# Kernel tuning notes

Hardware: AMD Instinct MI355X
Metric: run time of the kernel (lower is better)

Reference implementation:

```python
import jax, jax.numpy as jnp
import numpy as np
from jax import lax

WIN = 9
LOSS_WEIGHT = 1.0

def _box_sum(x, win):
    return lax.reduce_window(x, 0.0, lax.add,
                             window_dimensions=(1, 1, win, win, win),
                             window_strides=(1, 1, 1, 1, 1),
                             padding='SAME')

def setup_inputs() -> dict:
    key = jax.random.key(0)
    k1, k2 = jax.random.split(key)
    shape = (2, 1, 160, 192, 160)
    predict = jax.random.uniform(k1, shape, dtype=jnp.float32)
    target = jax.random.uniform(k2, shape, dtype=jnp.float32)
    return {"predict": predict, "target": target}

def reference(predict, target):
    Ii, Ji = target, predict
    win = WIN
    win_size = float(win ** 3)

    I_sum = _box_sum(Ii, win)
    J_sum = _box_sum(Ji, win)
    I2_sum = _box_sum(Ii * Ii, win)
    J2_sum = _box_sum(Ji * Ji, win)
    IJ_sum = _box_sum(Ii * Ji, win)

    u_I = I_sum / win_size
    u_J = J_sum / win_size
    cross = IJ_sum - u_J * I_sum - u_I * J_sum + u_I * u_J * win_size
    I_var = I2_sum - 2.0 * u_I * I_sum + u_I * u_I * win_size
    J_var = J2_sum - 2.0 * u_J * J_sum + u_J * u_J * win_size
    cc = cross * cross / (I_var * J_var + 1e-05)
    loss = 1.0 - jnp.mean(cc)
    return loss * LOSS_WEIGHT
```

## Files before the change

kernel.cpp:

```cpp
#include <hip/hip_runtime.h>
#include <hip/hip_fp16.h>


#define NX 160
#define NY 192
#define NZ 160
#define NB 2
#define SLICE (NX * NY)
#define VOL   (SLICE * NZ)
#define TOTAL (VOL * NB)

#define TX 32
#define TY 16
#define ZC 5
#define GXT (NX / TX)
#define GYT (NY / TY)
#define GZT (NZ / ZC)
#define NBLK (GXT * GYT * GZT * NB)

#define HY 24
#define ZRS 40
#define ZQQ (HY * ZRS + 8)
#define RRS 40
#define RQQ (HY * RRS + 8)
#define SRS 40
#define SQQ (TY * SRS + 8)
#define INV729 (1.0f / 729.0f)

__device__ __forceinline__ void lds_barrier() {
    asm volatile("s_waitcnt lgkmcnt(0)" ::: "memory");
    __builtin_amdgcn_s_barrier();
}

__device__ __forceinline__ float4 f4add(float4 a, float4 b) {
    return make_float4(a.x + b.x, a.y + b.y, a.z + b.z, a.w + b.w);
}
__device__ __forceinline__ float4 f4sub(float4 a, float4 b) {
    return make_float4(a.x - b.x, a.y - b.y, a.z - b.z, a.w - b.w);
}
__device__ __forceinline__ float4 f4mul(float4 a, float4 b) {
    return make_float4(a.x * b.x, a.y * b.y, a.z * b.z, a.w * b.w);
}

union U8 { uint4 u; __half2 h[4]; };

__device__ __forceinline__ U8 ld8(const __half* p) {
    U8 r; r.u = *(const uint4*)p; return r;
}
__device__ __forceinline__ void st8(__half* p, const U8& v) {
    *(uint4*)p = v.u;
}

__global__ __launch_bounds__(256) void ncc_main(
    const float* __restrict__ J_pred,
    const float* __restrict__ I_targ,
    float* __restrict__ partial)
{
    const int tid = threadIdx.x;

    const int lin = blockIdx.x;
    const int s   = (lin & 7) * (NBLK / 8) + (lin >> 3);
    const int bx  = s % GXT;
    const int r1  = s / GXT;
    const int by  = r1 % GYT;
    const int r2  = r1 / GYT;
    const int zc  = r2 % GZT;
    const int b   = r2 / GZT;

    const int x0 = bx * TX;
    const int y0 = by * TY;
    const int z0 = zc * ZC;

    __shared__ __align__(16) __half Zq[5 * ZQQ];
    __shared__ __align__(16) __half Rq[5 * RQQ];
    __shared__ float redbuf[4];
    __half* const Sq = Zq;

    const bool is_col = (tid < 240);
    const int  crow = tid / 10;
    const int  cxg  = tid - crow * 10;
    const int  gy = y0 - 4 + crow;
    const int  gx = x0 - 4 + cxg * 4;
    const bool vxy = is_col && ((unsigned)gy < (unsigned)NY) && (gx >= 0) && (gx <= NX - 4);
    const size_t cbase = (size_t)b * VOL + (vxy ? (size_t)(gy * NX + gx) : 0);
    const float* const baseI = I_targ + cbase;
    const float* const baseJ = J_pred + cbase;

    const float4 f40 = make_float4(0.f, 0.f, 0.f, 0.f);
    float4 rS0 = f40, rS1 = f40, rS2 = f40, rS3 = f40, rS4 = f40;

#pragma unroll 3
    for (int ss = 0; ss < 9; ++ss) {
        const int z = z0 - 5 + ss;
        float4 aI = f40, aJ = f40;
        if (vxy && (unsigned)z < (unsigned)NZ) {
            aI = *(const float4*)(baseI + (size_t)z * SLICE);
            aJ = *(const float4*)(baseJ + (size_t)z * SLICE);
        }
        rS0 = f4add(rS0, aI);
        rS1 = f4add(rS1, aJ);
        rS2 = f4add(rS2, f4mul(aI, aI));
        rS3 = f4add(rS3, f4mul(aJ, aJ));
        rS4 = f4add(rS4, f4mul(aI, aJ));
    }

    float4 nIa = f40, nJa = f40, nIs = f40, nJs = f40;
    if (vxy) {
        const int za = z0 + 4;
        nIa = *(const float4*)(baseI + (size_t)za * SLICE);
        nJa = *(const float4*)(baseJ + (size_t)za * SLICE);
        const int zs = z0 - 5;
        if (zs >= 0) {
            nIs = *(const float4*)(baseI + (size_t)zs * SLICE);
            nJs = *(const float4*)(baseJ + (size_t)zs * SLICE);
        }
    }

    const int ty  = tid >> 4;
    const int tx2 = tid & 15;
    float acc = 0.f;

#pragma unroll 1
    for (int so = 0; so < ZC; ++so) {
        rS0 = f4add(rS0, f4sub(nIa, nIs));
        rS1 = f4add(rS1, f4sub(nJa, nJs));
        rS2 = f4add(rS2, f4sub(f4mul(nIa, nIa), f4mul(nIs, nIs)));
        rS3 = f4add(rS3, f4sub(f4mul(nJa, nJa), f4mul(nJs, nJs)));
        rS4 = f4add(rS4, f4sub(f4mul(nIa, nJa), f4mul(nIs, nJs)));

        nIa = f40; nJa = f40; nIs = f40; nJs = f40;
        if (so < ZC - 1 && vxy) {
            const int za = z0 + 5 + so;
            if (za < NZ) {
                nIa = *(const float4*)(baseI + (size_t)za * SLICE);
                nJa = *(const float4*)(baseJ + (size_t)za * SLICE);
            }
            const int zs = z0 + so - 4;
            if (zs >= 0) {
                nIs = *(const float4*)(baseI + (size_t)zs * SLICE);
                nJs = *(const float4*)(baseJ + (size_t)zs * SLICE);
            }
        }

        if (is_col) {
            const int o = crow * ZRS + cxg * 4;
            union { uint2 u; __half2 h[2]; } pk;
            pk.h[0] = __float22half2_rn(make_float2(rS0.x, rS0.y));
            pk.h[1] = __float22half2_rn(make_float2(rS0.z, rS0.w));
            *(uint2*)&Zq[0 * ZQQ + o] = pk.u;
            pk.h[0] = __float22half2_rn(make_float2(rS1.x, rS1.y));
            pk.h[1] = __float22half2_rn(make_float2(rS1.z, rS1.w));
            *(uint2*)&Zq[1 * ZQQ + o] = pk.u;
            pk.h[0] = __float22half2_rn(make_float2(rS2.x, rS2.y));
            pk.h[1] = __float22half2_rn(make_float2(rS2.z, rS2.w));
            *(uint2*)&Zq[2 * ZQQ + o] = pk.u;
            pk.h[0] = __float22half2_rn(make_float2(rS3.x, rS3.y));
            pk.h[1] = __float22half2_rn(make_float2(rS3.z, rS3.w));
            *(uint2*)&Zq[3 * ZQQ + o] = pk.u;
            pk.h[0] = __float22half2_rn(make_float2(rS4.x, rS4.y));
            pk.h[1] = __float22half2_rn(make_float2(rS4.z, rS4.w));
            *(uint2*)&Zq[4 * ZQQ + o] = pk.u;
        }
        lds_barrier();

        if (tid < 240) {
            const int q   = tid / 48;
            const int rem = tid - q * 48;
            const int row = rem >> 1;
            const int h   = rem & 1;
            const __half* src = &Zq[q * ZQQ + row * ZRS + h * 16];
            float c[24];
#pragma unroll
            for (int g = 0; g < 3; ++g) {
                U8 v = ld8(src + g * 8);
#pragma unroll
                for (int j = 0; j < 4; ++j) {
                    const float2 f = __half22float2(v.h[j]);
                    c[g * 8 + j * 2 + 0] = f.x;
                    c[g * 8 + j * 2 + 1] = f.y;
                }
            }
            float sx = c[0] + c[1] + c[2] + c[3] + c[4]
                     + c[5] + c[6] + c[7] + c[8];
            float o[16];
            o[0] = sx;
#pragma unroll
            for (int i = 1; i < 16; ++i) { sx += c[i + 8] - c[i - 1]; o[i] = sx; }
            __half* dst = &Rq[q * RQQ + row * RRS + h * 16];
#pragma unroll
            for (int g = 0; g < 2; ++g) {
                U8 w;
#pragma unroll
                for (int j = 0; j < 4; ++j)
                    w.h[j] = __float22half2_rn(make_float2(o[g * 8 + j * 2],
                                                           o[g * 8 + j * 2 + 1]));
                st8(dst + g * 8, w);
            }
        }
        lds_barrier();

        if (tid < 80) {
            const int q  = tid / 16;
            const int rm = tid & 15;
            const int xg = rm >> 2;
            const int q4 = rm & 3;
            const __half* rb = &Rq[q * RQQ + (q4 * 4) * RRS + xg * 8];
            __half* sb = &Sq[q * SQQ + (q4 * 4) * SRS + xg * 8];
            U8 sum = ld8(rb);
#pragma unroll
            for (int k = 1; k < 9; ++k) {
                const U8 t = ld8(rb + k * RRS);
#pragma unroll
                for (int j = 0; j < 4; ++j) sum.h[j] = __hadd2(sum.h[j], t.h[j]);
            }
            st8(sb, sum);
#pragma unroll
            for (int i = 1; i < 4; ++i) {
                const U8 nw = ld8(rb + (i + 8) * RRS);
                const U8 od = ld8(rb + (i - 1) * RRS);
#pragma unroll
                for (int j = 0; j < 4; ++j)
                    sum.h[j] = __hadd2(sum.h[j], __hsub2(nw.h[j], od.h[j]));
                st8(sb + i * SRS, sum);
            }
        }
        lds_barrier();

        {
            const int o = ty * SRS + tx2 * 2;
            const float2 S0 = __half22float2(*(const __half2*)&Sq[0 * SQQ + o]);
            const float2 S1 = __half22float2(*(const __half2*)&Sq[1 * SQQ + o]);
            const float2 S2 = __half22float2(*(const __half2*)&Sq[2 * SQQ + o]);
            const float2 S3 = __half22float2(*(const __half2*)&Sq[3 * SQQ + o]);
            const float2 S4 = __half22float2(*(const __half2*)&Sq[4 * SQQ + o]);
            {
                const float cross = S4.x - S0.x * S1.x * INV729;
                const float Iv    = S2.x - S0.x * S0.x * INV729;
                const float Jv    = S3.x - S1.x * S1.x * INV729;
                acc += (cross * cross) / (Iv * Jv + 1e-5f);
            }
            {
                const float cross = S4.y - S0.y * S1.y * INV729;
                const float Iv    = S2.y - S0.y * S0.y * INV729;
                const float Jv    = S3.y - S1.y * S1.y * INV729;
                acc += (cross * cross) / (Iv * Jv + 1e-5f);
            }
        }
        lds_barrier();
    }

#pragma unroll
    for (int off = 32; off > 0; off >>= 1) acc += __shfl_down(acc, off);
    __syncthreads();
    if ((tid & 63) == 0) redbuf[tid >> 6] = acc;
    __syncthreads();
    if (tid == 0) partial[s] = redbuf[0] + redbuf[1] + redbuf[2] + redbuf[3];
}

__global__ __launch_bounds__(256) void ncc_final(
    const float* __restrict__ partial, float* __restrict__ out)
{
    __shared__ float sm[256];
    const int tid = threadIdx.x;
    float v = 0.f;
    for (int i = tid; i < NBLK; i += 256) v += partial[i];
    sm[tid] = v;
    __syncthreads();
#pragma unroll
    for (int w = 128; w > 0; w >>= 1) {
        if (tid < w) sm[tid] += sm[tid + w];
        __syncthreads();
    }
    if (tid == 0) out[0] = 1.0f - sm[0] * (1.0f / (float)TOTAL);
}

extern "C" void kernel_launch(void* const* d_in, const int* in_sizes, int n_in,
                              void* d_out, int out_size, void* d_ws, size_t ws_size,
                              hipStream_t stream)
{
    const float* predict = (const float*)d_in[0];
    const float* target  = (const float*)d_in[1];
    float* partial = (float*)d_ws;

    ncc_main<<<dim3(NBLK), 256, 0, stream>>>(predict, target, partial);
    ncc_final<<<1, 256, 0, stream>>>(partial, (float*)d_out);
}
```

Before: 59.99 us.

## Make z-sum and y-pass LDS staging wave-private to drop two block barriers

Each wave now owns six halo rows for the z-sum staging and four output rows for the y-pass, in a wave-private LDS region. This turns two of the four per-slice block barriers into wave-local lgkmcnt waits, keeping only the barrier around the shared x-pass buffer. The running z-sums of squares also switch to FMA and a difference-times-sum form to trim VALU work. The cost is more LDS footprint, and the result depends on lockstep execution within a wave for the private buffers to stay correct.

```diff
diff --git a/kernel.cpp b/kernel.cpp
--- a/kernel.cpp
+++ b/kernel.cpp
@@ -18,19 +18,24 @@
 #define GZT (NZ / ZC)
 #define NBLK (GXT * GYT * GZT * NB)
 
-#define HY 24
-#define ZRS 40
-#define ZQQ (HY * ZRS + 8)
+#define WROWS 6
+#define ZQS 48
+#define ZQP (WROWS * ZQS + 8)
+#define ZPRIV (5 * ZQP)
+#define ZPRIVP 1504
+#define SQS 40
+#define SQP (4 * SQS + 8)
 #define RRS 40
-#define RQQ (HY * RRS + 8)
-#define SRS 40
-#define SQQ (TY * SRS + 8)
+#define RQQ (24 * RRS + 8)
 #define INV729 (1.0f / 729.0f)
 
 __device__ __forceinline__ void lds_barrier() {
     asm volatile("s_waitcnt lgkmcnt(0)" ::: "memory");
     __builtin_amdgcn_s_barrier();
 }
+__device__ __forceinline__ void lds_fence() {
+    asm volatile("s_waitcnt lgkmcnt(0)" ::: "memory");
+}
 
 __device__ __forceinline__ float4 f4add(float4 a, float4 b) {
     return make_float4(a.x + b.x, a.y + b.y, a.z + b.z, a.w + b.w);
@@ -41,9 +46,12 @@
 __device__ __forceinline__ float4 f4mul(float4 a, float4 b) {
     return make_float4(a.x * b.x, a.y * b.y, a.z * b.z, a.w * b.w);
 }
+__device__ __forceinline__ float4 f4fma(float4 a, float4 b, float4 c) {
+    return make_float4(fmaf(a.x, b.x, c.x), fmaf(a.y, b.y, c.y),
+                       fmaf(a.z, b.z, c.z), fmaf(a.w, b.w, c.w));
+}
 
 union U8 { uint4 u; __half2 h[4]; };
-
 __device__ __forceinline__ U8 ld8(const __half* p) {
     U8 r; r.u = *(const uint4*)p; return r;
 }
@@ -56,7 +64,9 @@
     const float* __restrict__ I_targ,
     float* __restrict__ partial)
 {
-    const int tid = threadIdx.x;
+    const int tid  = threadIdx.x;
+    const int wave = tid >> 6;
+    const int lane = tid & 63;
 
     const int lin = blockIdx.x;
     const int s   = (lin & 7) * (NBLK / 8) + (lin >> 3);
@@ -71,16 +81,17 @@
     const int y0 = by * TY;
     const int z0 = zc * ZC;
 
-    __shared__ __align__(16) __half Zq[5 * ZQQ];
+    __shared__ __align__(16) __half ZS[4 * ZPRIVP];
     __shared__ __align__(16) __half Rq[5 * RQQ];
     __shared__ float redbuf[4];
-    __half* const Sq = Zq;
-
-    const bool is_col = (tid < 240);
-    const int  crow = tid / 10;
-    const int  cxg  = tid - crow * 10;
-    const int  gy = y0 - 4 + crow;
-    const int  gx = x0 - 4 + cxg * 4;
+    __half* const ZW = &ZS[wave * ZPRIVP];
+
+    const bool is_col = (lane < 60);
+    const int  rl  = lane / 10;
+    const int  xg  = lane - rl * 10;
+    const int  row = wave * WROWS + rl;
+    const int  gy  = y0 - 4 + row;
+    const int  gx  = x0 - 4 + xg * 4;
     const bool vxy = is_col && ((unsigned)gy < (unsigned)NY) && (gx >= 0) && (gx <= NX - 4);
     const size_t cbase = (size_t)b * VOL + (vxy ? (size_t)(gy * NX + gx) : 0);
     const float* const baseI = I_targ + cbase;
@@ -99,9 +110,9 @@
         }
         rS0 = f4add(rS0, aI);
         rS1 = f4add(rS1, aJ);
-        rS2 = f4add(rS2, f4mul(aI, aI));
-        rS3 = f4add(rS3, f4mul(aJ, aJ));
-        rS4 = f4add(rS4, f4mul(aI, aJ));
+        rS2 = f4fma(aI, aI, rS2);
+        rS3 = f4fma(aJ, aJ, rS3);
+        rS4 = f4fma(aI, aJ, rS4);
     }
 
     float4 nIa = f40, nJa = f40, nIs = f40, nJs = f40;
@@ -122,11 +133,15 @@
 
 #pragma unroll 1
     for (int so = 0; so < ZC; ++so) {
-        rS0 = f4add(rS0, f4sub(nIa, nIs));
-        rS1 = f4add(rS1, f4sub(nJa, nJs));
-        rS2 = f4add(rS2, f4sub(f4mul(nIa, nIa), f4mul(nIs, nIs)));
-        rS3 = f4add(rS3, f4sub(f4mul(nJa, nJa), f4mul(nJs, nJs)));
-        rS4 = f4add(rS4, f4sub(f4mul(nIa, nJa), f4mul(nIs, nJs)));
+        {
+            const float4 dI = f4sub(nIa, nIs), pI = f4add(nIa, nIs);
+            const float4 dJ = f4sub(nJa, nJs), pJ = f4add(nJa, nJs);
+            rS0 = f4add(rS0, dI);
+            rS1 = f4add(rS1, dJ);
+            rS2 = f4fma(dI, pI, rS2);
+            rS3 = f4fma(dJ, pJ, rS3);
+            rS4 = f4add(rS4, f4sub(f4mul(nIa, nJa), f4mul(nIs, nJs)));
+        }
 
         nIa = f40; nJa = f40; nIs = f40; nJs = f40;
         if (so < ZC - 1 && vxy) {
@@ -143,32 +158,31 @@
         }
 
         if (is_col) {
-            const int o = crow * ZRS + cxg * 4;
+            const int o = rl * ZQS + xg * 4;
             union { uint2 u; __half2 h[2]; } pk;
             pk.h[0] = __float22half2_rn(make_float2(rS0.x, rS0.y));
             pk.h[1] = __float22half2_rn(make_float2(rS0.z, rS0.w));
-            *(uint2*)&Zq[0 * ZQQ + o] = pk.u;
+            *(uint2*)&ZW[0 * ZQP + o] = pk.u;
             pk.h[0] = __float22half2_rn(make_float2(rS1.x, rS1.y));
             pk.h[1] = __float22half2_rn(make_float2(rS1.z, rS1.w));
-            *(uint2*)&Zq[1 * ZQQ + o] = pk.u;
+            *(uint2*)&ZW[1 * ZQP + o] = pk.u;
             pk.h[0] = __float22half2_rn(make_float2(rS2.x, rS2.y));
             pk.h[1] = __float22half2_rn(make_float2(rS2.z, rS2.w));
-            *(uint2*)&Zq[2 * ZQQ + o] = pk.u;
+            *(uint2*)&ZW[2 * ZQP + o] = pk.u;
             pk.h[0] = __float22half2_rn(make_float2(rS3.x, rS3.y));
             pk.h[1] = __float22half2_rn(make_float2(rS3.z, rS3.w));
-            *(uint2*)&Zq[3 * ZQQ + o] = pk.u;
+            *(uint2*)&ZW[3 * ZQP + o] = pk.u;
             pk.h[0] = __float22half2_rn(make_float2(rS4.x, rS4.y));
             pk.h[1] = __float22half2_rn(make_float2(rS4.z, rS4.w));
-            *(uint2*)&Zq[4 * ZQQ + o] = pk.u;
-        }
-        lds_barrier();
-
-        if (tid < 240) {
-            const int q   = tid / 48;
-            const int rem = tid - q * 48;
-            const int row = rem >> 1;
+            *(uint2*)&ZW[4 * ZQP + o] = pk.u;
+        }
+        lds_fence();
+
+        if (lane < 60) {
+            const int rem = lane - rl * 10;
+            const int q   = rem >> 1;
             const int h   = rem & 1;
-            const __half* src = &Zq[q * ZQQ + row * ZRS + h * 16];
+            const __half* src = &ZW[q * ZQP + rl * ZQS + h * 16];
             float c[24];
 #pragma unroll
             for (int g = 0; g < 3; ++g) {
@@ -199,13 +213,11 @@
         }
         lds_barrier();
 
-        if (tid < 80) {
-            const int q  = tid / 16;
-            const int rm = tid & 15;
-            const int xg = rm >> 2;
-            const int q4 = rm & 3;
-            const __half* rb = &Rq[q * RQQ + (q4 * 4) * RRS + xg * 8];
-            __half* sb = &Sq[q * SQQ + (q4 * 4) * SRS + xg * 8];
+        if (lane < 20) {
+            const int q3 = lane >> 2;
+            const int x3 = lane & 3;
+            const __half* rb = &Rq[q3 * RQQ + (wave * 4) * RRS + x3 * 8];
+            __half* sb = &ZW[q3 * SQP + x3 * 8];
             U8 sum = ld8(rb);
 #pragma unroll
             for (int k = 1; k < 9; ++k) {
@@ -221,18 +233,18 @@
 #pragma unroll
                 for (int j = 0; j < 4; ++j)
                     sum.h[j] = __hadd2(sum.h[j], __hsub2(nw.h[j], od.h[j]));
-                st8(sb + i * SRS, sum);
-            }
-        }
-        lds_barrier();
+                st8(sb + i * SQS, sum);
+            }
+        }
+        lds_fence();
 
         {
-            const int o = ty * SRS + tx2 * 2;
-            const float2 S0 = __half22float2(*(const __half2*)&Sq[0 * SQQ + o]);
-            const float2 S1 = __half22float2(*(const __half2*)&Sq[1 * SQQ + o]);
-            const float2 S2 = __half22float2(*(const __half2*)&Sq[2 * SQQ + o]);
-            const float2 S3 = __half22float2(*(const __half2*)&Sq[3 * SQQ + o]);
-            const float2 S4 = __half22float2(*(const __half2*)&Sq[4 * SQQ + o]);
+            const int o = (ty & 3) * SQS + tx2 * 2;
+            const float2 S0 = __half22float2(*(const __half2*)&ZW[0 * SQP + o]);
+            const float2 S1 = __half22float2(*(const __half2*)&ZW[1 * SQP + o]);
+            const float2 S2 = __half22float2(*(const __half2*)&ZW[2 * SQP + o]);
+            const float2 S3 = __half22float2(*(const __half2*)&ZW[3 * SQP + o]);
+            const float2 S4 = __half22float2(*(const __half2*)&ZW[4 * SQP + o]);
             {
                 const float cross = S4.x - S0.x * S1.x * INV729;
                 const float Iv    = S2.x - S0.x * S0.x * INV729;
```

New measurement: 61.41 us. 1.02x slower.
